# Optimization experiments

Hardware: AMD Instinct MI355X
Metric: run time of the kernel (lower is better)

## Reference

```python
import jax, jax.numpy as jnp
import numpy as np

# 2^22-point radix-2 DIT FFT; NOTE the original code applies tf.abs at EVERY
# recursion level (not just the top), so each butterfly stage is followed by a
# magnitude + recomplexification. We reproduce that exact (non-standard) math.
N = 1 << 22
STAGES = 22


def _bitrev_perm(n, bits):
    # vectorized bit-reversal permutation (the order induced by the even/odd
    # decimation inputs[0::2] / inputs[1::2] recursion)
    x = np.arange(n)
    r = np.zeros(n, dtype=np.int64)
    for b in range(bits):
        r = (r << 1) | ((x >> b) & 1)
    return r


_PERM = jnp.asarray(_bitrev_perm(N, STAGES))


def setup_inputs() -> dict:
    key = jax.random.key(0)
    x = jax.random.normal(key, (N,), dtype=jnp.float32)
    return {"x": x}


def reference(x):
    # base case of the recursion: length-1 leaves are the bit-reversed inputs
    y = x[_PERM].astype(jnp.complex64)
    for s in range(1, STAGES + 1):  # fixed log2(N) stages, not a data loop
        m = 1 << s                  # sub-FFT size at this stage
        yb = y.reshape(N // m, m)   # [num_blocks, m]
        e = yb[:, : m // 2]         # 'even' sub-results
        o = yb[:, m // 2:]          # 'odd'  sub-results
        # twiddles W(m, k) = exp(-2*pi*i*k/m)
        tw = jnp.exp(
            jnp.complex64(-2j * np.pi) * jnp.arange(m // 2, dtype=jnp.float32) / m
        ).astype(jnp.complex64)
        t = tw[None, :] * o
        # butterfly then tf.abs (applied at every level in the original)
        mag = jnp.abs(jnp.concatenate([e + t, e - t], axis=1)).reshape(N)
        y = mag.astype(jnp.complex64) if s < STAGES else mag
    return y  # float32 magnitudes, shape [N]
```

## Files before the change

kernel.cpp:

```cpp
#include <hip/hip_runtime.h>
#include <math.h>


#define NBITS 22
#define RSQ2 0.70710678118654752440f

__device__ __forceinline__ float hsqrt(float x) { return __builtin_amdgcn_sqrtf(x); }

__device__ __forceinline__ void bf(float& e, float& o, float c, float s) {
    float rp = fmaf(c, o, e);
    float rm = fmaf(-c, o, e);
    float im = s * o;
    float im2 = im * im;
    e = hsqrt(fmaf(rp, rp, im2));
    o = hsqrt(fmaf(rm, rm, im2));
}
__device__ __forceinline__ void bf0(float& e, float& o) {
    float a = e + o, b = e - o;
    e = fabsf(a); o = fabsf(b);
}
__device__ __forceinline__ void bfq(float& e, float& o) {
    float h = hsqrt(fmaf(e, e, o * o));
    e = h; o = h;
}

__device__ __constant__ float KC[16] = {
    1.f, 0.980785280f, 0.923879533f, 0.831469612f, 0.707106781f, 0.555570233f,
    0.382683432f, 0.195090322f, 0.f, -0.195090322f, -0.382683432f, -0.555570233f,
    -0.707106781f, -0.831469612f, -0.923879533f, -0.980785280f };
__device__ __constant__ float KS[16] = {
    0.f, 0.195090322f, 0.382683432f, 0.555570233f, 0.707106781f, 0.831469612f,
    0.923879533f, 0.980785280f, 1.f, 0.980785280f, 0.923879533f, 0.831469612f,
    0.707106781f, 0.555570233f, 0.382683432f, 0.195090322f };

template <int L>
__device__ __forceinline__ void radixN(float* v, float c, float s) {
    float ca[L], sa[L];
    ca[L - 1] = c; sa[L - 1] = s;
#pragma unroll
    for (int a = L - 1; a > 0; --a) {
        ca[a - 1] = fmaf(-2.f * sa[a], sa[a], 1.f);
        sa[a - 1] = 2.f * sa[a] * ca[a];
    }
#pragma unroll
    for (int a = 0; a < L; ++a) {
        const int half = 1 << a;
#pragma unroll
        for (int d = 0; d < half; ++d) {
            const int k = d << (4 - a);
            float cd = fmaf(ca[a], KC[k], -sa[a] * KS[k]);
            float sd = fmaf(sa[a], KC[k],  ca[a] * KS[k]);
#pragma unroll
            for (int g = d; g < (1 << L); g += 2 * half)
                bf(v[g], v[g + half], cd, sd);
        }
    }
}

__device__ __forceinline__ void radix8z(float v[8]) {
    bf0(v[0], v[1]); bf0(v[2], v[3]); bf0(v[4], v[5]); bf0(v[6], v[7]);
    bf0(v[0], v[2]); bf0(v[4], v[6]);
    bfq(v[1], v[3]); bfq(v[5], v[7]);
    bf0(v[0], v[4]);
    bf(v[1], v[5], RSQ2, RSQ2);
    bfq(v[2], v[6]);
    bf(v[3], v[7], -RSQ2, RSQ2);
}

__device__ __forceinline__ unsigned apad(unsigned q) { return q + 4u * (q >> 8); }
__device__ __forceinline__ unsigned bpad(unsigned t, unsigned li) {
    return 20u * t + li + 8u * (t >> 5);
}

__global__ __launch_bounds__(256, 4) void fft_perm(const float* __restrict__ x,
                                                   float* __restrict__ y) {
    __shared__ float lds[64 * 65];
    const unsigned tid = threadIdx.x;
    const unsigned C0 = (blockIdx.x & 31) * 64;
    const unsigned B0 = (blockIdx.x >> 5) * 64;
    const unsigned qi = tid & 15, rr = tid >> 4;

#pragma unroll
    for (int k = 0; k < 4; ++k) {
        unsigned r = rr + 16u * k;
        unsigned a = __brev(C0 + r) >> (32 - 11);
        float4 f = *(const float4*)(x + a * 2048u + B0 + 4u * qi);
        float* p = &lds[r * 65u + 4u * qi];
        p[0] = f.x; p[1] = f.y; p[2] = f.z; p[3] = f.w;
    }
    __syncthreads();

    float v[8];
#pragma unroll
    for (int q = 0; q < 2; ++q) {
        unsigned task = tid + 256u * q;
        unsigned c = task >> 3, grp = task & 7;
#pragma unroll
        for (int j = 0; j < 8; ++j) v[j] = lds[(grp * 8u + j) * 65u + c];
        radix8z(v);
        unsigned pr = __brev(B0 + c) >> (32 - 11);
        float* dst = y + pr * 2048u + C0 + grp * 8u;
        *(float4*)(dst)     = make_float4(v[0], v[1], v[2], v[3]);
        *(float4*)(dst + 4) = make_float4(v[4], v[5], v[6], v[7]);
    }
}

__global__ __launch_bounds__(256, 2) void fft_low(float* __restrict__ y) {
    __shared__ float lds[8316];
    const unsigned t = threadIdx.x;
    const unsigned base = blockIdx.x * 8192u;
    float v[32];

    {
        const float4* __restrict__ src4 = (const float4*)(y + base);
#pragma unroll
        for (int k = 0; k < 8; ++k) {
            unsigned kk = ((unsigned)k + blockIdx.x) & 7u;
            float4 f = src4[t + 256u * kk];
            *(float4*)&lds[apad(4u * (t + 256u * kk))] = f;
        }
    }
    __syncthreads();

    const unsigned lo = t & 7, hi = t >> 3;
    {
#pragma unroll
        for (int j = 0; j < 32; ++j) v[j] = lds[apad(lo + 8u * j + 256u * hi)];
        float r = (float)lo * (1.f / 256.f);
        radixN<5>(v, __builtin_amdgcn_cosf(r), __builtin_amdgcn_sinf(r));
#pragma unroll
        for (int j = 0; j < 32; ++j) lds[apad(lo + 8u * j + 256u * hi)] = v[j];
    }
    __syncthreads();

    {
#pragma unroll
        for (int j = 0; j < 32; ++j) v[j] = lds[apad(t + 256u * j)];
        float r = (float)t * (1.f / 8192.f);
        radixN<5>(v, __builtin_amdgcn_cosf(r), __builtin_amdgcn_sinf(r));
        float* dst = y + base + t;
#pragma unroll
        for (int j = 0; j < 32; ++j) {
            unsigned jj = ((unsigned)j + blockIdx.x) & 31u;
            dst[256u * jj] = v[jj];
        }
    }
}

__global__ __launch_bounds__(256, 2) void fft_high(float* __restrict__ y) {
    __shared__ float lds[10356];
    const unsigned tt = threadIdx.x;
    const unsigned low0 = blockIdx.x * 16u;
    float4* __restrict__ Y4 = (float4*)y;
    const unsigned lq = tt & 3, tv = tt >> 2;
    float v[32];

#pragma unroll
    for (int k = 0; k < 8; ++k) {
        unsigned t = tv + 64u * (((unsigned)k + blockIdx.x) & 7u);
        float4 f = Y4[(low0 >> 2) + lq + 2048u * t];
        *(float4*)&lds[bpad(t, 4u * lq)] = f;
    }
    __syncthreads();

    const unsigned li = tt & 15, u5 = tt >> 4;
    {
#pragma unroll
        for (int j = 0; j < 32; ++j) v[j] = lds[bpad(32u * u5 + j, li)];
        float r = (float)(low0 + li) * (1.f / 262144.f);
        radixN<5>(v, __builtin_amdgcn_cosf(r), __builtin_amdgcn_sinf(r));
#pragma unroll
        for (int j = 0; j < 32; ++j) lds[bpad(32u * u5 + j, li)] = v[j];
    }
    __syncthreads();

#pragma unroll
    for (int b = 0; b < 2; ++b) {
        const unsigned t0 = 2u * u5 + b;
        float* w = v + 16 * b;
#pragma unroll
        for (int j = 0; j < 16; ++j) w[j] = lds[bpad(t0 + 32u * j, li)];
        float r = ((float)(low0 + li) + 8192.f * (float)t0) * (1.f / 4194304.f);
        radixN<4>(w, __builtin_amdgcn_cosf(r), __builtin_amdgcn_sinf(r));
#pragma unroll
        for (int j = 0; j < 16; ++j) lds[bpad(t0 + 32u * j, li)] = w[j];
    }
    __syncthreads();

#pragma unroll
    for (int k = 0; k < 8; ++k) {
        unsigned t = tv + 64u * (((unsigned)k + 5u + blockIdx.x) & 7u);
        Y4[(low0 >> 2) + lq + 2048u * t] = *(float4*)&lds[bpad(t, 4u * lq)];
    }
}

extern "C" void kernel_launch(void* const* d_in, const int* in_sizes, int n_in,
                              void* d_out, int out_size, void* d_ws, size_t ws_size,
                              hipStream_t stream) {
    const float* x = (const float*)d_in[0];
    float* out = (float*)d_out;

    fft_perm<<<dim3(1024), dim3(256), 0, stream>>>(x, out);
    fft_low<<<dim3(512), dim3(256), 0, stream>>>(out);
    fft_high<<<dim3(512), dim3(256), 0, stream>>>(out);
}
```

Baseline: 103.1 us.

## Use 512-thread blocks with smaller per-thread radix passes across all three FFT kernels

All three kernels move from 256 to 512 threads per block. Each thread now does radix-16/radix-4/radix-2 passes instead of radix-32, so it holds 16 values instead of 32, which cuts register pressure and should allow higher occupancy. fft_low now loads its first pass directly from global memory into registers rather than staging through LDS first. fft_high replaces its float4 staging with scalar strided loads and stores, uses a new LDS padding scheme, and adds an extra radix-2 pass. The risks are more LDS round trips and synchronisation points per block, and less coalesced global accesses in fft_high.

```diff
diff --git a/kernel.cpp b/kernel.cpp
--- a/kernel.cpp
+++ b/kernel.cpp
@@ -2,10 +2,11 @@
 #include <math.h>
 
 
-#define NBITS 22
 #define RSQ2 0.70710678118654752440f
 
 __device__ __forceinline__ float hsqrt(float x) { return __builtin_amdgcn_sqrtf(x); }
+__device__ __forceinline__ float cosr(float r) { return __builtin_amdgcn_cosf(r); }
+__device__ __forceinline__ float sinr(float r) { return __builtin_amdgcn_sinf(r); }
 
 __device__ __forceinline__ void bf(float& e, float& o, float c, float s) {
     float rp = fmaf(c, o, e);
@@ -67,12 +68,10 @@
     bf(v[3], v[7], -RSQ2, RSQ2);
 }
 
-__device__ __forceinline__ unsigned apad(unsigned q) { return q + 4u * (q >> 8); }
-__device__ __forceinline__ unsigned bpad(unsigned t, unsigned li) {
-    return 20u * t + li + 8u * (t >> 5);
-}
-
-__global__ __launch_bounds__(256, 4) void fft_perm(const float* __restrict__ x,
+__device__ __forceinline__ unsigned apad(unsigned q) { return q + (q >> 5); }
+__device__ __forceinline__ unsigned bmap(unsigned t, unsigned li) { return t * 17u + li; }
+
+__global__ __launch_bounds__(512, 8) void fft_perm(const float* __restrict__ x,
                                                    float* __restrict__ y) {
     __shared__ float lds[64 * 65];
     const unsigned tid = threadIdx.x;
@@ -81,8 +80,8 @@
     const unsigned qi = tid & 15, rr = tid >> 4;
 
 #pragma unroll
-    for (int k = 0; k < 4; ++k) {
-        unsigned r = rr + 16u * k;
+    for (int k = 0; k < 2; ++k) {
+        unsigned r = rr + 32u * k;
         unsigned a = __brev(C0 + r) >> (32 - 11);
         float4 f = *(const float4*)(x + a * 2048u + B0 + 4u * qi);
         float* p = &lds[r * 65u + 4u * qi];
@@ -91,106 +90,101 @@
     __syncthreads();
 
     float v[8];
-#pragma unroll
-    for (int q = 0; q < 2; ++q) {
-        unsigned task = tid + 256u * q;
-        unsigned c = task >> 3, grp = task & 7;
-#pragma unroll
-        for (int j = 0; j < 8; ++j) v[j] = lds[(grp * 8u + j) * 65u + c];
-        radix8z(v);
-        unsigned pr = __brev(B0 + c) >> (32 - 11);
-        float* dst = y + pr * 2048u + C0 + grp * 8u;
-        *(float4*)(dst)     = make_float4(v[0], v[1], v[2], v[3]);
-        *(float4*)(dst + 4) = make_float4(v[4], v[5], v[6], v[7]);
-    }
-}
-
-__global__ __launch_bounds__(256, 2) void fft_low(float* __restrict__ y) {
-    __shared__ float lds[8316];
+    const unsigned c = tid >> 3, grp = tid & 7;
+#pragma unroll
+    for (int j = 0; j < 8; ++j) v[j] = lds[(grp * 8u + j) * 65u + c];
+    radix8z(v);
+    unsigned pr = __brev(B0 + c) >> (32 - 11);
+    float* dst = y + pr * 2048u + C0 + grp * 8u;
+    *(float4*)(dst)     = make_float4(v[0], v[1], v[2], v[3]);
+    *(float4*)(dst + 4) = make_float4(v[4], v[5], v[6], v[7]);
+}
+
+__global__ __launch_bounds__(512, 4) void fft_low(float* __restrict__ y) {
+    __shared__ float lds[8447];
     const unsigned t = threadIdx.x;
     const unsigned base = blockIdx.x * 8192u;
-    float v[32];
-
-    {
-        const float4* __restrict__ src4 = (const float4*)(y + base);
-#pragma unroll
-        for (int k = 0; k < 8; ++k) {
-            unsigned kk = ((unsigned)k + blockIdx.x) & 7u;
-            float4 f = src4[t + 256u * kk];
-            *(float4*)&lds[apad(4u * (t + 256u * kk))] = f;
-        }
-    }
-    __syncthreads();
-
-    const unsigned lo = t & 7, hi = t >> 3;
-    {
-#pragma unroll
-        for (int j = 0; j < 32; ++j) v[j] = lds[apad(lo + 8u * j + 256u * hi)];
-        float r = (float)lo * (1.f / 256.f);
-        radixN<5>(v, __builtin_amdgcn_cosf(r), __builtin_amdgcn_sinf(r));
-#pragma unroll
-        for (int j = 0; j < 32; ++j) lds[apad(lo + 8u * j + 256u * hi)] = v[j];
-    }
-    __syncthreads();
-
-    {
-#pragma unroll
-        for (int j = 0; j < 32; ++j) v[j] = lds[apad(t + 256u * j)];
-        float r = (float)t * (1.f / 8192.f);
-        radixN<5>(v, __builtin_amdgcn_cosf(r), __builtin_amdgcn_sinf(r));
-        float* dst = y + base + t;
-#pragma unroll
-        for (int j = 0; j < 32; ++j) {
-            unsigned jj = ((unsigned)j + blockIdx.x) & 31u;
-            dst[256u * jj] = v[jj];
-        }
-    }
-}
-
-__global__ __launch_bounds__(256, 2) void fft_high(float* __restrict__ y) {
-    __shared__ float lds[10356];
+    float v[16];
+
+    {
+        const unsigned lo = t & 7, h = t >> 3;
+        const float* src = y + base + lo + 128u * h;
+#pragma unroll
+        for (int j = 0; j < 16; ++j) v[j] = src[8u * j];
+        float r = (float)lo * (1.f / 128.f);
+        radixN<4>(v, cosr(r), sinr(r));
+#pragma unroll
+        for (int j = 0; j < 16; ++j) lds[apad(lo + 8u * j + 128u * h)] = v[j];
+    }
+    __syncthreads();
+
+    {
+        const unsigned m = t & 127, g = t >> 7;
+#pragma unroll
+        for (int j = 0; j < 16; ++j) v[j] = lds[apad(m + 128u * j + 2048u * g)];
+        float r = (float)m * (1.f / 2048.f);
+        radixN<4>(v, cosr(r), sinr(r));
+#pragma unroll
+        for (int j = 0; j < 16; ++j) lds[apad(m + 128u * j + 2048u * g)] = v[j];
+    }
+    __syncthreads();
+
+#pragma unroll
+    for (int w = 0; w < 4; ++w) {
+        const unsigned c = t + 512u * w;
+        float u4[4];
+#pragma unroll
+        for (int j = 0; j < 4; ++j) u4[j] = lds[apad(c + 2048u * j)];
+        float r = (float)c * (1.f / 8192.f);
+        radixN<2>(u4, cosr(r), sinr(r));
+#pragma unroll
+        for (int j = 0; j < 4; ++j) y[base + c + 2048u * j] = u4[j];
+    }
+}
+
+__global__ __launch_bounds__(512, 4) void fft_high(float* __restrict__ y) {
+    __shared__ float lds[17 * 511 + 16];
     const unsigned tt = threadIdx.x;
     const unsigned low0 = blockIdx.x * 16u;
-    float4* __restrict__ Y4 = (float4*)y;
-    const unsigned lq = tt & 3, tv = tt >> 2;
-    float v[32];
-
-#pragma unroll
-    for (int k = 0; k < 8; ++k) {
-        unsigned t = tv + 64u * (((unsigned)k + blockIdx.x) & 7u);
-        float4 f = Y4[(low0 >> 2) + lq + 2048u * t];
-        *(float4*)&lds[bpad(t, 4u * lq)] = f;
-    }
-    __syncthreads();
-
-    const unsigned li = tt & 15, u5 = tt >> 4;
-    {
-#pragma unroll
-        for (int j = 0; j < 32; ++j) v[j] = lds[bpad(32u * u5 + j, li)];
-        float r = (float)(low0 + li) * (1.f / 262144.f);
-        radixN<5>(v, __builtin_amdgcn_cosf(r), __builtin_amdgcn_sinf(r));
-#pragma unroll
-        for (int j = 0; j < 32; ++j) lds[bpad(32u * u5 + j, li)] = v[j];
-    }
-    __syncthreads();
-
-#pragma unroll
-    for (int b = 0; b < 2; ++b) {
-        const unsigned t0 = 2u * u5 + b;
-        float* w = v + 16 * b;
-#pragma unroll
-        for (int j = 0; j < 16; ++j) w[j] = lds[bpad(t0 + 32u * j, li)];
-        float r = ((float)(low0 + li) + 8192.f * (float)t0) * (1.f / 4194304.f);
-        radixN<4>(w, __builtin_amdgcn_cosf(r), __builtin_amdgcn_sinf(r));
-#pragma unroll
-        for (int j = 0; j < 16; ++j) lds[bpad(t0 + 32u * j, li)] = w[j];
-    }
-    __syncthreads();
-
-#pragma unroll
-    for (int k = 0; k < 8; ++k) {
-        unsigned t = tv + 64u * (((unsigned)k + 5u + blockIdx.x) & 7u);
-        Y4[(low0 >> 2) + lq + 2048u * t] = *(float4*)&lds[bpad(t, 4u * lq)];
+    const unsigned li = tt & 15;
+    const float lowf = (float)(low0 + li);
+    float v[16];
+
+    {
+        const unsigned u = tt >> 4;
+        const float* src = y + low0 + li + 131072u * u;
+#pragma unroll
+        for (int j = 0; j < 16; ++j) v[j] = src[8192u * j];
+        float r = lowf * (1.f / 131072.f);
+        radixN<4>(v, cosr(r), sinr(r));
+#pragma unroll
+        for (int j = 0; j < 16; ++j) lds[bmap(16u * u + j, li)] = v[j];
+    }
+    __syncthreads();
+
+    {
+        const unsigned idx = tt >> 4;
+        const unsigned t0 = idx & 15, b = idx >> 4;
+#pragma unroll
+        for (int j = 0; j < 16; ++j)
+            v[j] = lds[bmap(t0 + 16u * j + 256u * b, li)];
+        float r = fmaf(8192.f, (float)t0, lowf) * (1.f / 2097152.f);
+        radixN<4>(v, cosr(r), sinr(r));
+#pragma unroll
+        for (int j = 0; j < 16; ++j)
+            lds[bmap(t0 + 16u * j + 256u * b, li)] = v[j];
+    }
+    __syncthreads();
+
+#pragma unroll
+    for (int w = 0; w < 8; ++w) {
+        unsigned tau = (tt >> 4) + 32u * w;
+        float e = lds[bmap(tau, li)];
+        float o = lds[bmap(tau + 256u, li)];
+        float r = fmaf(8192.f, (float)tau, lowf) * (1.f / 4194304.f);
+        bf(e, o, cosr(r), sinr(r));
+        y[low0 + li + 8192u * tau]          = e;
+        y[low0 + li + 8192u * (tau + 256u)] = o;
     }
 }
 
@@ -200,7 +194,7 @@
     const float* x = (const float*)d_in[0];
     float* out = (float*)d_out;
 
-    fft_perm<<<dim3(1024), dim3(256), 0, stream>>>(x, out);
-    fft_low<<<dim3(512), dim3(256), 0, stream>>>(out);
-    fft_high<<<dim3(512), dim3(256), 0, stream>>>(out);
-}
+    fft_perm<<<dim3(1024), dim3(512), 0, stream>>>(x, out);
+    fft_low<<<dim3(512), dim3(512), 0, stream>>>(out);
+    fft_high<<<dim3(512), dim3(512), 0, stream>>>(out);
+}
```

New measurement: 99.90 us. -3.1%, faster.
